# Performance work log

Measured on AMD Instinct MI355X. Metric: run time of the kernel, lower is better.

The kernel has to match this reference:

```python
import jax, jax.numpy as jnp
import numpy as np

B, T, N = 512, 512, 128   # batch, timesteps, driving series
M = 64                    # LSTM hidden size
UNITS = 64                # attention units


def setup_inputs() -> dict:
    key = jax.random.key(0)
    ks = jax.random.split(key, 9)
    s = lambda fan_in: 1.0 / np.sqrt(fan_in)
    return {
        "x": jax.random.normal(ks[0], (B, T, N), jnp.float32),
        "hidden_state": jax.random.normal(ks[1], (B, M), jnp.float32),
        "cell_state": jax.random.normal(ks[2], (B, M), jnp.float32),
        # Dense(units) applied to x permuted to (B, N, T): kernel contracts T
        "w1_kernel": jax.random.normal(ks[3], (T, UNITS), jnp.float32) * s(T),
        "w1_bias": jnp.zeros((UNITS,), jnp.float32),
        # Dense(units) applied to query (B, N, 2M)
        "w2_kernel": jax.random.normal(ks[4], (2 * M, UNITS), jnp.float32) * s(2 * M),
        "w2_bias": jnp.zeros((UNITS,), jnp.float32),
        # Dense(1) scoring
        "v_kernel": jax.random.normal(ks[5], (UNITS, 1), jnp.float32) * s(UNITS),
        "v_bias": jnp.zeros((1,), jnp.float32),
    }


def reference(x, hidden_state, cell_state, w1_kernel, w1_bias,
              w2_kernel, w2_bias, v_kernel, v_bias):
    # query: (B, 2M) -> broadcast over the N feature axis (RepeatVector)
    query = jnp.concatenate([hidden_state, cell_state], axis=-1)
    q_proj = query @ w2_kernel + w2_bias                    # (B, UNITS)
    x_perm = jnp.transpose(x, (0, 2, 1))                    # (B, N, T)
    score = jnp.tanh(x_perm @ w1_kernel + w1_bias + q_proj[:, None, :])  # (B, N, UNITS)
    score = score @ v_kernel + v_bias                       # (B, N, 1)
    score = jnp.transpose(score, (0, 2, 1))                 # (B, 1, N)
    attention_weights = jax.nn.softmax(score, axis=-1)      # (B, 1, N)
    context_vector = jnp.sum(attention_weights * x, axis=-1)  # (B, T)
    return context_vector, attention_weights
```

## Files before the change

kernel.cpp:

```cpp
#include <hip/hip_runtime.h>
#include <hip/hip_bf16.h>

namespace {

constexpr int kB = 512, kT = 512, kN = 128, kM = 64, kU = 64;
constexpr int TT = 64;

__device__ __forceinline__ float fast_tanh(float x) {
  return 1.0f - 2.0f / (__expf(2.0f * x) + 1.0f);
}

struct Smem {
  float xs[TT][kN];
  float w1s[TT][kU];
  float qp[kU];
  float sred[16][kN + 1];
  float sn[kN];
  float aw[kN];
};

__global__ __launch_bounds__(256) void fused_kernel(
    const float* __restrict__ x,
    const float* __restrict__ hs,
    const float* __restrict__ cs,
    const float* __restrict__ w1,
    const float* __restrict__ w1b,
    const float* __restrict__ w2,
    const float* __restrict__ w2b,
    const float* __restrict__ vk,
    const float* __restrict__ vb,
    float* __restrict__ ctx_out,
    float* __restrict__ aw_out)
{
  __shared__ Smem s;
  const int b = blockIdx.x;
  const int tid = threadIdx.x;

  if (tid < kU) {
    float a0 = w2b[tid] + w1b[tid];
    for (int k = 0; k < kM; ++k)
      a0 = fmaf(hs[(size_t)b * kM + k], w2[k * kU + tid], a0);
    for (int k = 0; k < kM; ++k)
      a0 = fmaf(cs[(size_t)b * kM + k], w2[(kM + k) * kU + tid], a0);
    s.qp[tid] = a0;
  }

  const int n0 = (tid >> 4) * 8;
  const int u0 = (tid & 15) * 4;

  float acc[8][4];
#pragma unroll
  for (int j = 0; j < 8; ++j)
#pragma unroll
    for (int i = 0; i < 4; ++i) acc[j][i] = 0.f;

  for (int t0 = 0; t0 < kT; t0 += TT) {
    __syncthreads();
    {
      const float4* xp = (const float4*)(x + ((size_t)b * kT + t0) * kN);
#pragma unroll
      for (int i = 0; i < 8; ++i) {
        int idx = tid + i * 256;
        *(float4*)&s.xs[idx >> 5][(idx & 31) * 4] = xp[idx];
      }
      const float4* wp = (const float4*)(w1 + (size_t)t0 * kU);
#pragma unroll
      for (int i = 0; i < 4; ++i) {
        int idx = tid + i * 256;
        *(float4*)&s.w1s[idx >> 4][(idx & 15) * 4] = wp[idx];
      }
    }
    __syncthreads();

#pragma unroll 4
    for (int tt = 0; tt < TT; ++tt) {
      float xv[8], wv[4];
      *(float4*)&xv[0] = *(const float4*)&s.xs[tt][n0];
      *(float4*)&xv[4] = *(const float4*)&s.xs[tt][n0 + 4];
      *(float4*)&wv[0] = *(const float4*)&s.w1s[tt][u0];
#pragma unroll
      for (int j = 0; j < 8; ++j)
#pragma unroll
        for (int i = 0; i < 4; ++i)
          acc[j][i] = fmaf(xv[j], wv[i], acc[j][i]);
    }
  }

  float qv[4], vv[4];
#pragma unroll
  for (int i = 0; i < 4; ++i) {
    qv[i] = s.qp[u0 + i];
    vv[i] = vk[u0 + i];
  }
#pragma unroll
  for (int j = 0; j < 8; ++j) {
    float p = 0.f;
#pragma unroll
    for (int i = 0; i < 4; ++i)
      p = fmaf(fast_tanh(acc[j][i] + qv[i]), vv[i], p);
    s.sred[tid & 15][n0 + j] = p;
  }
  __syncthreads();
  if (tid < kN) {
    float v = vb[0];
#pragma unroll
    for (int g = 0; g < 16; ++g) v += s.sred[g][tid];
    s.sn[tid] = v;
  }
  __syncthreads();

  if (tid < 64) {
    float s0 = s.sn[tid], s1 = s.sn[tid + 64];
    float m = fmaxf(s0, s1);
#pragma unroll
    for (int off = 32; off > 0; off >>= 1) m = fmaxf(m, __shfl_xor(m, off));
    float e0 = __expf(s0 - m), e1 = __expf(s1 - m);
    float se = e0 + e1;
#pragma unroll
    for (int off = 32; off > 0; off >>= 1) se += __shfl_xor(se, off);
    float inv = 1.0f / se;
    float a0 = e0 * inv, a1 = e1 * inv;
    s.aw[tid] = a0;
    s.aw[tid + 64] = a1;
    aw_out[(size_t)b * kN + tid] = a0;
    aw_out[(size_t)b * kN + tid + 64] = a1;
  }
  __syncthreads();

  const int lr = tid & 3;
  const int qrow = tid >> 2;
  for (int rg = 0; rg < 8; ++rg) {
    const int r = rg * 64 + qrow;
    const float4* xp = (const float4*)(x + ((size_t)b * kT + r) * kN);
    float a = 0.f;
#pragma unroll
    for (int k = 0; k < 8; ++k) {
      int i = lr + k * 4;
      float4 v = xp[i];
      const float* w = &s.aw[i * 4];
      a = fmaf(v.x, w[0], a);
      a = fmaf(v.y, w[1], a);
      a = fmaf(v.z, w[2], a);
      a = fmaf(v.w, w[3], a);
    }
    a += __shfl_xor(a, 1);
    a += __shfl_xor(a, 2);
    if (lr == 0) ctx_out[(size_t)b * kT + r] = a;
  }
}

}

extern "C" void kernel_launch(void* const* d_in, const int* in_sizes, int n_in,
                              void* d_out, int out_size, void* d_ws, size_t ws_size,
                              hipStream_t stream) {
  const float* x   = (const float*)d_in[0];
  const float* hs  = (const float*)d_in[1];
  const float* cs  = (const float*)d_in[2];
  const float* w1  = (const float*)d_in[3];
  const float* w1b = (const float*)d_in[4];
  const float* w2  = (const float*)d_in[5];
  const float* w2b = (const float*)d_in[6];
  const float* vk  = (const float*)d_in[7];
  const float* vb  = (const float*)d_in[8];

  float* out = (float*)d_out;
  float* ctx = out;
  float* awo = out + (size_t)kB * kT;

  hipLaunchKernelGGL(fused_kernel, dim3(kB), dim3(256), 0, stream,
                     x, hs, cs, w1, w1b, w2, w2b, vk, vb, ctx, awo);
}
```

Measured before the change: 248.2 us.

## Use split-bf16 MFMA for score GEMM and split context into separate kernel

```diff
diff --git a/kernel.cpp b/kernel.cpp
--- a/kernel.cpp
+++ b/kernel.cpp
@@ -5,21 +5,46 @@
 
 constexpr int kB = 512, kT = 512, kN = 128, kM = 64, kU = 64;
 constexpr int TT = 64;
+constexpr int SX = 68;
+
+typedef __attribute__((ext_vector_type(8))) short short8;
+typedef __attribute__((ext_vector_type(16))) float f32x16;
+
+__device__ __forceinline__ unsigned pack_hl(float v) {
+  unsigned u = __float_as_uint(v);
+  unsigned hs = (u + 0x7fffu + ((u >> 16) & 1u)) >> 16;
+  float lo = v - __uint_as_float(hs << 16);
+  unsigned ul = __float_as_uint(lo);
+  unsigned ls = (ul + 0x7fffu + ((ul >> 16) & 1u)) >> 16;
+  return (hs << 16) | (ls & 0xffffu);
+}
 
 __device__ __forceinline__ float fast_tanh(float x) {
   return 1.0f - 2.0f / (__expf(2.0f * x) + 1.0f);
 }
 
-struct Smem {
-  float xs[TT][kN];
-  float w1s[TT][kU];
-  float qp[kU];
-  float sred[16][kN + 1];
+union FragU { unsigned u[4]; short8 s; };
+
+__device__ __forceinline__ void unpack_hl(const unsigned* p, short8& hi, short8& lo) {
+  FragU H, L;
+#pragma unroll
+  for (int j = 0; j < 4; ++j) {
+    unsigned a = p[2 * j], b = p[2 * j + 1];
+    H.u[j] = (a >> 16) | (b & 0xffff0000u);
+    L.u[j] = (a & 0xffffu) | (b << 16);
+  }
+  hi = H.s; lo = L.s;
+}
+
+struct __align__(16) SmemS {
+  unsigned xsT[kN * SX];
+  unsigned w1T[kU * SX];
+  float qpart[8][kU];
+  float sred[2][kN];
   float sn[kN];
-  float aw[kN];
 };
 
-__global__ __launch_bounds__(256) void fused_kernel(
+__global__ __launch_bounds__(512, 4) void score_kernel(
     const float* __restrict__ x,
     const float* __restrict__ hs,
     const float* __restrict__ cs,
@@ -28,85 +53,119 @@
     const float* __restrict__ w2,
     const float* __restrict__ w2b,
     const float* __restrict__ vk,
-    const float* __restrict__ vb,
-    float* __restrict__ ctx_out,
     float* __restrict__ aw_out)
 {
-  __shared__ Smem s;
+  __shared__ SmemS s;
   const int b = blockIdx.x;
   const int tid = threadIdx.x;
-
-  if (tid < kU) {
-    float a0 = w2b[tid] + w1b[tid];
-    for (int k = 0; k < kM; ++k)
-      a0 = fmaf(hs[(size_t)b * kM + k], w2[k * kU + tid], a0);
-    for (int k = 0; k < kM; ++k)
-      a0 = fmaf(cs[(size_t)b * kM + k], w2[(kM + k) * kU + tid], a0);
-    s.qp[tid] = a0;
-  }
-
-  const int n0 = (tid >> 4) * 8;
-  const int u0 = (tid & 15) * 4;
-
-  float acc[8][4];
+  const int l = tid & 63;
+  const int w = tid >> 6;
+
+  {
+    const int u = tid & 63, kg = tid >> 6;
+    float a0 = 0.f;
+#pragma unroll
+    for (int j = 0; j < 16; ++j) {
+      int k = kg * 16 + j;
+      float qv = (k < kM) ? hs[(size_t)b * kM + k] : cs[(size_t)b * kM + (k - kM)];
+      a0 = fmaf(qv, w2[k * kU + u], a0);
+    }
+    s.qpart[kg][u] = a0;
+  }
+
+  const int xn = l + 64 * (w & 1);
+  const int xts = (w >> 1) * 16;
+  const int wu = l;
+  const int wts = w * 8;
+
+  const int kh = l >> 5;
+  const int mrow = (w & 3) * 32 + (l & 31);
+  const int urow = (w >> 2) * 32 + (l & 31);
+
+  f32x16 acc;
+#pragma unroll
+  for (int i = 0; i < 16; ++i) acc[i] = 0.f;
+
+  float rx[16], rw[8];
+#pragma unroll
+  for (int j = 0; j < 16; ++j)
+    rx[j] = x[((size_t)b * kT + xts + j) * kN + xn];
 #pragma unroll
   for (int j = 0; j < 8; ++j)
-#pragma unroll
-    for (int i = 0; i < 4; ++i) acc[j][i] = 0.f;
+    rw[j] = w1[(size_t)(wts + j) * kU + wu];
 
   for (int t0 = 0; t0 < kT; t0 += TT) {
     __syncthreads();
     {
-      const float4* xp = (const float4*)(x + ((size_t)b * kT + t0) * kN);
-#pragma unroll
-      for (int i = 0; i < 8; ++i) {
-        int idx = tid + i * 256;
-        *(float4*)&s.xs[idx >> 5][(idx & 31) * 4] = xp[idx];
-      }
-      const float4* wp = (const float4*)(w1 + (size_t)t0 * kU);
-#pragma unroll
-      for (int i = 0; i < 4; ++i) {
-        int idx = tid + i * 256;
-        *(float4*)&s.w1s[idx >> 4][(idx & 15) * 4] = wp[idx];
-      }
+      unsigned px[16];
+#pragma unroll
+      for (int j = 0; j < 16; ++j) px[j] = pack_hl(rx[j]);
+#pragma unroll
+      for (int jj = 0; jj < 4; ++jj)
+        *(uint4*)&s.xsT[xn * SX + xts + 4 * jj] =
+            make_uint4(px[4 * jj], px[4 * jj + 1], px[4 * jj + 2], px[4 * jj + 3]);
+      unsigned pw[8];
+#pragma unroll
+      for (int j = 0; j < 8; ++j) pw[j] = pack_hl(rw[j]);
+#pragma unroll
+      for (int jj = 0; jj < 2; ++jj)
+        *(uint4*)&s.w1T[wu * SX + wts + 4 * jj] =
+            make_uint4(pw[4 * jj], pw[4 * jj + 1], pw[4 * jj + 2], pw[4 * jj + 3]);
     }
     __syncthreads();
-
-#pragma unroll 4
-    for (int tt = 0; tt < TT; ++tt) {
-      float xv[8], wv[4];
-      *(float4*)&xv[0] = *(const float4*)&s.xs[tt][n0];
-      *(float4*)&xv[4] = *(const float4*)&s.xs[tt][n0 + 4];
-      *(float4*)&wv[0] = *(const float4*)&s.w1s[tt][u0];
+    if (t0 + TT < kT) {
+#pragma unroll
+      for (int j = 0; j < 16; ++j)
+        rx[j] = x[((size_t)b * kT + t0 + TT + xts + j) * kN + xn];
 #pragma unroll
       for (int j = 0; j < 8; ++j)
-#pragma unroll
-        for (int i = 0; i < 4; ++i)
-          acc[j][i] = fmaf(xv[j], wv[i], acc[j][i]);
-    }
-  }
-
-  float qv[4], vv[4];
-#pragma unroll
-  for (int i = 0; i < 4; ++i) {
-    qv[i] = s.qp[u0 + i];
-    vv[i] = vk[u0 + i];
-  }
-#pragma unroll
-  for (int j = 0; j < 8; ++j) {
-    float p = 0.f;
-#pragma unroll
-    for (int i = 0; i < 4; ++i)
-      p = fmaf(fast_tanh(acc[j][i] + qv[i]), vv[i], p);
-    s.sred[tid & 15][n0 + j] = p;
+        rw[j] = w1[(size_t)(t0 + TT + wts + j) * kU + wu];
+    }
+
+#pragma unroll
+    for (int ss = 0; ss < 4; ++ss) {
+      unsigned ra[8];
+      const unsigned* pa = &s.xsT[mrow * SX + 16 * ss + 8 * kh];
+      *(uint4*)&ra[0] = *(const uint4*)pa;
+      *(uint4*)&ra[4] = *(const uint4*)(pa + 4);
+      short8 ah, al;
+      unpack_hl(ra, ah, al);
+
+      unsigned rb[8];
+      const unsigned* pb = &s.w1T[urow * SX + 16 * ss + 8 * kh];
+      *(uint4*)&rb[0] = *(const uint4*)pb;
+      *(uint4*)&rb[4] = *(const uint4*)(pb + 4);
+      short8 bh, bl;
+      unpack_hl(rb, bh, bl);
+
+      acc = __builtin_amdgcn_mfma_f32_32x32x16_bf16(ah, bh, acc, 0, 0, 0);
+      acc = __builtin_amdgcn_mfma_f32_32x32x16_bf16(ah, bl, acc, 0, 0, 0);
+      acc = __builtin_amdgcn_mfma_f32_32x32x16_bf16(al, bh, acc, 0, 0, 0);
+    }
+  }
+
+  float qpu = w2b[urow] + w1b[urow];
+#pragma unroll
+  for (int g = 0; g < 8; ++g) qpu += s.qpart[g][urow];
+  const float vu = vk[urow];
+
+  float pr[16];
+#pragma unroll
+  for (int r = 0; r < 16; ++r)
+    pr[r] = fast_tanh(acc[r] + qpu) * vu;
+#pragma unroll
+  for (int off = 1; off < 32; off <<= 1)
+#pragma unroll
+    for (int r = 0; r < 16; ++r)
+      pr[r] += __shfl_xor(pr[r], off);
+
+  if ((l & 31) == 0) {
+#pragma unroll
+    for (int r = 0; r < 16; ++r)
+      s.sred[w >> 2][(w & 3) * 32 + (r & 3) + 8 * (r >> 2) + 4 * kh] = pr[r];
   }
   __syncthreads();
-  if (tid < kN) {
-    float v = vb[0];
-#pragma unroll
-    for (int g = 0; g < 16; ++g) v += s.sred[g][tid];
-    s.sn[tid] = v;
-  }
+  if (tid < kN) s.sn[tid] = s.sred[0][tid] + s.sred[1][tid];
   __syncthreads();
 
   if (tid < 64) {
@@ -119,33 +178,42 @@
 #pragma unroll
     for (int off = 32; off > 0; off >>= 1) se += __shfl_xor(se, off);
     float inv = 1.0f / se;
-    float a0 = e0 * inv, a1 = e1 * inv;
-    s.aw[tid] = a0;
-    s.aw[tid + 64] = a1;
-    aw_out[(size_t)b * kN + tid] = a0;
-    aw_out[(size_t)b * kN + tid + 64] = a1;
-  }
+    aw_out[(size_t)b * kN + tid] = e0 * inv;
+    aw_out[(size_t)b * kN + tid + 64] = e1 * inv;
+  }
+}
+
+__global__ __launch_bounds__(256) void context_kernel(
+    const float* __restrict__ x,
+    const float* __restrict__ aw_in,
+    float* __restrict__ ctx)
+{
+  __shared__ float aw[kN];
+  const int b = blockIdx.x >> 2;
+  const int seg = blockIdx.x & 3;
+  if (threadIdx.x < kN) aw[threadIdx.x] = aw_in[(size_t)b * kN + threadIdx.x];
   __syncthreads();
 
-  const int lr = tid & 3;
-  const int qrow = tid >> 2;
-  for (int rg = 0; rg < 8; ++rg) {
-    const int r = rg * 64 + qrow;
+  const int lr = threadIdx.x & 3;
+  const int row = threadIdx.x >> 2;
+#pragma unroll
+  for (int rg = 0; rg < 2; ++rg) {
+    const int r = seg * 128 + rg * 64 + row;
     const float4* xp = (const float4*)(x + ((size_t)b * kT + r) * kN);
     float a = 0.f;
 #pragma unroll
     for (int k = 0; k < 8; ++k) {
       int i = lr + k * 4;
       float4 v = xp[i];
-      const float* w = &s.aw[i * 4];
-      a = fmaf(v.x, w[0], a);
-      a = fmaf(v.y, w[1], a);
-      a = fmaf(v.z, w[2], a);
-      a = fmaf(v.w, w[3], a);
+      const float* wa = &aw[i * 4];
+      a = fmaf(v.x, wa[0], a);
+      a = fmaf(v.y, wa[1], a);
+      a = fmaf(v.z, wa[2], a);
+      a = fmaf(v.w, wa[3], a);
     }
     a += __shfl_xor(a, 1);
     a += __shfl_xor(a, 2);
-    if (lr == 0) ctx_out[(size_t)b * kT + r] = a;
+    if (lr == 0) ctx[(size_t)b * kT + r] = a;
   }
 }
 
@@ -162,12 +230,13 @@
   const float* w2  = (const float*)d_in[5];
   const float* w2b = (const float*)d_in[6];
   const float* vk  = (const float*)d_in[7];
-  const float* vb  = (const float*)d_in[8];
 
   float* out = (float*)d_out;
   float* ctx = out;
   float* awo = out + (size_t)kB * kT;
 
-  hipLaunchKernelGGL(fused_kernel, dim3(kB), dim3(256), 0, stream,
-                     x, hs, cs, w1, w1b, w2, w2b, vk, vb, ctx, awo);
-}
+  hipLaunchKernelGGL(score_kernel, dim3(kB), dim3(512), 0, stream,
+                     x, hs, cs, w1, w1b, w2, w2b, vk, awo);
+  hipLaunchKernelGGL(context_kernel, dim3(kB * 4), dim3(256), 0, stream,
+                     x, awo, ctx);
+}
```

Result: faster. 228.1 us (-8.1%).
